# Kernel optimization log

Hardware: AMD Instinct MI355X
Metric: run time of the kernel (lower is better)

## Reference

```python
import jax, jax.numpy as jnp
import numpy as np

B, N, D, E, H = 4, 2048, 512, 16, 1024
CAP = max(4, min(N, int(N * 2.0 / E)))   # eval capacity_factor = 2.0 -> 256
EPS = 1e-9
THRESH = 0.2  # second_threshold_eval


def setup_inputs() -> dict:
    key = jax.random.key(0)
    ks = jax.random.split(key, 10)
    f32 = jnp.float32
    return {
        "X": jax.random.normal(ks[0], (B, N, D), f32),
        "probs": jax.random.uniform(ks[1], (B, N), f32),
        "W1": jax.random.normal(ks[2], (D, D), f32) * (1.0 / np.sqrt(D)),
        "b1": jnp.zeros((D,), f32),
        "Wg": jax.random.normal(ks[3], (D, E), f32),  # Top2Gating uses randn init
        "We1": jax.random.normal(ks[4], (E, D, H), f32) * (1.0 / np.sqrt(D)),
        "We2": jax.random.normal(ks[5], (E, H, D), f32) * (1.0 / np.sqrt(H)),
        "W3": jax.random.normal(ks[6], (D, 4), f32) * (1.0 / np.sqrt(D)),
        "b3": jnp.zeros((4,), f32),
        "W4": jax.random.normal(ks[7], (4, 1), f32) * 0.5,
        "b4": jnp.zeros((1,), f32),
    }


def top2_gating(x, Wg, probs):
    # x: [B, N, D] -> raw gates [B, N, E]
    raw = jax.nn.softmax(jnp.einsum('bnd,de->bne', x, Wg), axis=-1)
    dt = raw.dtype

    gate1 = jnp.max(raw, axis=-1)
    idx1 = jnp.argmax(raw, axis=-1)
    mask1 = jax.nn.one_hot(idx1, E, dtype=dt)
    density_proxy = raw

    raw_wo1 = raw * (1.0 - mask1)
    gate2 = jnp.max(raw_wo1, axis=-1)
    idx2 = jnp.argmax(raw_wo1, axis=-1)
    mask2 = jax.nn.one_hot(idx2, E, dtype=dt)

    denom = gate1 + gate2 + EPS
    gate1 = gate1 / denom
    gate2 = gate2 / denom

    # load-balancing loss (computed but wrapper discards it)
    density1 = jnp.mean(mask1, axis=-2)
    loss = jnp.mean(jnp.mean(density_proxy, axis=-2) * density1) * float(E ** 2)

    # second policy == 'random'
    mask2 = mask2 * (probs < (gate2 / max(THRESH, EPS))).astype(dt)[..., None]

    # exclusive cumsum along the group dim gives position within each expert
    pos1 = (jnp.cumsum(mask1, axis=-2) - mask1) * mask1          # [B, N, E]
    mask1 = mask1 * (pos1 < float(CAP)).astype(dt)
    mask1_count = jnp.sum(mask1, axis=-2, keepdims=True)
    mask1_flat = jnp.sum(mask1, axis=-1)                          # [B, N]
    pos1_flat = jnp.sum(pos1, axis=-1)
    gate1 = gate1 * mask1_flat

    pos2 = ((jnp.cumsum(mask2, axis=-2) - mask2) + mask1_count) * mask2
    mask2 = mask2 * (pos2 < float(CAP)).astype(dt)
    mask2_flat = jnp.sum(mask2, axis=-1)
    pos2_flat = jnp.sum(pos2, axis=-1)
    gate2 = gate2 * mask2_flat

    # safe one-hot: out-of-range positions map to all-zeros (jax.nn.one_hot semantics)
    oh_p1 = jax.nn.one_hot(pos1_flat.astype(jnp.int32), CAP, dtype=dt)
    oh_p2 = jax.nn.one_hot(pos2_flat.astype(jnp.int32), CAP, dtype=dt)
    oh_e1 = jax.nn.one_hot(idx1, E, dtype=dt)
    oh_e2 = jax.nn.one_hot(idx2, E, dtype=dt)

    combine = ((gate1 * mask1_flat)[..., None, None] * oh_e1[..., :, None] * oh_p1[..., None, :]
               + (gate2 * mask2_flat)[..., None, None] * oh_e2[..., :, None] * oh_p2[..., None, :])
    dispatch = (combine != 0).astype(dt)
    return dispatch, combine, loss


def reference(X, probs, W1, b1, Wg, We1, We2, W3, b3, W4, b4):
    h = X @ W1 + b1                                              # linear1
    dispatch, combine, loss = top2_gating(h, Wg, probs)
    exp_in = jnp.einsum('bnd,bnec->ebcd', h, dispatch)           # dispatch
    hid = jax.nn.leaky_relu(jnp.einsum('ebcd,edh->ebch', exp_in, We1))
    exp_out = jnp.einsum('ebch,ehd->ebcd', hid, We2)             # experts
    moe_out = jnp.einsum('bnec,ebcd->bnd', combine, exp_out)     # combine
    out = (moe_out @ W3 + b3) @ W4 + b4                          # hidden3 -> act3
    return out
```

## Files before the change

kernel.cpp:

```cpp
#include <hip/hip_runtime.h>
#include <hip/hip_bf16.h>

#define NB 4
#define NN 2048
#define ND 512
#define NE 16
#define NH 1024
#define CAP 256
#define NTOK (NB*NN)

typedef __attribute__((ext_vector_type(8))) short bf16x8;
typedef __attribute__((ext_vector_type(4))) float f32x4;
typedef __attribute__((ext_vector_type(8))) unsigned short u16x8;

__device__ __forceinline__ void gload16(const void* gsrc, void* lds) {
    __builtin_amdgcn_global_load_lds((const __attribute__((address_space(1))) void*)gsrc,
                                     (__attribute__((address_space(3))) void*)lds, 16, 0, 0);
}
__device__ __forceinline__ unsigned short f2bf(float f) {
    union { __hip_bfloat16 b; unsigned short u; } v; v.b = __float2bfloat16(f); return v.u;
}

__global__ __launch_bounds__(256) void prep_kernel(const float* __restrict__ W1,
                                                   const float* __restrict__ Wg,
                                                   unsigned short* __restrict__ W1B,
                                                   float* __restrict__ WcT,
                                                   float* __restrict__ zbuf) {
    const int tid = threadIdx.x;
    int bid = blockIdx.x;
    if (bid < 128) {
        const int w = tid >> 6, l = tid & 63;
        const int d = bid * 4 + w;
        float a0 = 0.f, a1 = 0.f, a2 = 0.f, a3 = 0.f, a4 = 0.f, a5 = 0.f, a6 = 0.f, a7 = 0.f;
        float a8 = 0.f, a9 = 0.f, aA = 0.f, aB = 0.f, aC = 0.f, aD = 0.f, aE = 0.f, aF = 0.f;
        #pragma unroll
        for (int ch = 0; ch < 8; ++ch) {
            float x = W1[(size_t)d * ND + ch * 64 + l];
            const float4* wg4 = (const float4*)(Wg + (size_t)(ch * 64 + l) * NE);
            float4 g0 = wg4[0], g1 = wg4[1], g2 = wg4[2], g3 = wg4[3];
            a0 = fmaf(x, g0.x, a0); a1 = fmaf(x, g0.y, a1); a2 = fmaf(x, g0.z, a2); a3 = fmaf(x, g0.w, a3);
            a4 = fmaf(x, g1.x, a4); a5 = fmaf(x, g1.y, a5); a6 = fmaf(x, g1.z, a6); a7 = fmaf(x, g1.w, a7);
            a8 = fmaf(x, g2.x, a8); a9 = fmaf(x, g2.y, a9); aA = fmaf(x, g2.z, aA); aB = fmaf(x, g2.w, aB);
            aC = fmaf(x, g3.x, aC); aD = fmaf(x, g3.y, aD); aE = fmaf(x, g3.z, aE); aF = fmaf(x, g3.w, aF);
        }
        float accs[16] = {a0, a1, a2, a3, a4, a5, a6, a7, a8, a9, aA, aB, aC, aD, aE, aF};
        #pragma unroll
        for (int off = 32; off >= 1; off >>= 1)
            #pragma unroll
            for (int e = 0; e < 16; ++e) accs[e] += __shfl_xor(accs[e], off);
        #pragma unroll
        for (int e = 0; e < 16; ++e)
            if (l == e) WcT[e * ND + d] = accs[e];
        return;
    }
    bid -= 128;
    {
        if (bid == 0) zbuf[tid] = 0.f;
        int dblk = bid >> 1, hblk = bid & 1;
        const float* src = W1 + (size_t)(dblk * 64) * ND + hblk * 256 + tid;
        unsigned short* dst = W1B + (size_t)(dblk * 512 + hblk * 256 + tid) * 64;
        float v[64];
        #pragma unroll
        for (int j = 0; j < 64; ++j) v[j] = src[(size_t)j * ND];
        #pragma unroll
        for (int q = 0; q < 8; ++q) {
            u16x8 o;
            #pragma unroll
            for (int j = 0; j < 8; ++j) o[j] = f2bf(v[q * 8 + j]);
            *(u16x8*)(dst + q * 8) = o;
        }
    }
}

__global__ __launch_bounds__(256) void gating_kernel(const float* __restrict__ X,
                                                     const float* __restrict__ WcT,
                                                     const float* __restrict__ probs,
                                                     unsigned short* __restrict__ Xbf,
                                                     int* __restrict__ idx1a, int* __restrict__ idx2a,
                                                     float* __restrict__ g1a, float* __restrict__ g2a,
                                                     int* __restrict__ pos1a, int* __restrict__ pos2a) {
    __shared__ float wc[NE * ND];
    const int tid = threadIdx.x;
    #pragma unroll
    for (int i = 0; i < 32; ++i) wc[tid + 256 * i] = WcT[tid + 256 * i];
    __syncthreads();
    const int w = tid >> 6, l = tid & 63;
    const float4* wc4 = (const float4*)wc;
    for (int j = 0; j < 4; ++j) {
        int tok = blockIdx.x * 16 + j * 4 + w;
        const float4* xrow = (const float4*)(X + (size_t)tok * ND);
        float4 x0 = xrow[l], x1 = xrow[l + 64];
        {
            ushort4 o0, o1;
            o0.x = f2bf(x0.x); o0.y = f2bf(x0.y); o0.z = f2bf(x0.z); o0.w = f2bf(x0.w);
            o1.x = f2bf(x1.x); o1.y = f2bf(x1.y); o1.z = f2bf(x1.z); o1.w = f2bf(x1.w);
            *(ushort4*)(Xbf + (size_t)tok * ND + 4 * l) = o0;
            *(ushort4*)(Xbf + (size_t)tok * ND + 256 + 4 * l) = o1;
        }
        float acc[NE];
        #pragma unroll
        for (int e = 0; e < NE; ++e) {
            float4 w0 = wc4[e * 128 + l], w1 = wc4[e * 128 + l + 64];
            acc[e] = x0.x * w0.x + x0.y * w0.y + x0.z * w0.z + x0.w * w0.w
                   + x1.x * w1.x + x1.y * w1.y + x1.z * w1.z + x1.w * w1.w;
        }
        #pragma unroll
        for (int off = 32; off >= 1; off >>= 1)
            #pragma unroll
            for (int e = 0; e < NE; ++e) acc[e] += __shfl_xor(acc[e], off);

        if (l == 0) {
            float m = acc[0];
            #pragma unroll
            for (int e = 1; e < NE; ++e) m = fmaxf(m, acc[e]);
            float raw[NE]; float s = 0.f;
            #pragma unroll
            for (int e = 0; e < NE; ++e) { raw[e] = expf(acc[e] - m); s += raw[e]; }
            #pragma unroll
            for (int e = 0; e < NE; ++e) raw[e] = raw[e] / s;
            int i1 = 0; float g1 = raw[0];
            #pragma unroll
            for (int e = 1; e < NE; ++e) if (raw[e] > g1) { g1 = raw[e]; i1 = e; }
            int i2 = -1; float g2 = -1.f;
            #pragma unroll
            for (int e = 0; e < NE; ++e) if (e != i1 && raw[e] > g2) { g2 = raw[e]; i2 = e; }
            float denom = g1 + g2 + 1e-9f;
            float g1n = g1 / denom, g2n = g2 / denom;
            bool flag = probs[tok] < (g2n / 0.2f);
            idx1a[tok] = i1;
            idx2a[tok] = flag ? i2 : -1;
            g1a[tok] = g1n;
            g2a[tok] = g2n;
            pos1a[tok] = -1;
            pos2a[tok] = -1;
        }
    }
}

__global__ __launch_bounds__(512) void scan_linear1_kernel(const int* __restrict__ idx1a,
                                                           const int* __restrict__ idx2a,
                                                           int* __restrict__ pos1a, int* __restrict__ pos2a,
                                                           int* __restrict__ slot_token,
                                                           const unsigned short* __restrict__ Xbf,
                                                           const unsigned short* __restrict__ W1B,
                                                           const float* __restrict__ b1,
                                                           unsigned short* __restrict__ hbf,
                                                           const float* __restrict__ We1,
                                                           unsigned short* __restrict__ We1B,
                                                           const float* __restrict__ We2,
                                                           const float* __restrict__ W3,
                                                           const float* __restrict__ W4,
                                                           float* __restrict__ u) {
    __shared__ char smem[65536];
    const int tid = threadIdx.x;
    const int w = tid >> 6, l = tid & 63;
    if (blockIdx.x < 64) {
        const int bb = blockIdx.x;
        const int b = bb >> 4, e = bb & 15;
        int* cnt1 = (int*)smem;
        int* cnt2 = cnt1 + 8;
        int* slot = slot_token + (e * NB + b) * CAP;
        const unsigned long long below = (l == 0) ? 0ull : ((1ull << l) - 1ull);
        const int base0 = w * 256;
        int c1 = 0, c2 = 0;
        #pragma unroll
        for (int it = 0; it < 4; ++it) {
            int n = base0 + it * 64 + l;
            c1 += __popcll(__ballot(idx1a[b * NN + n] == e));
            c2 += __popcll(__ballot(idx2a[b * NN + n] == e));
        }
        if (l == 0) { cnt1[w] = c1; cnt2[w] = c2; }
        __syncthreads();
        int b1c = 0, t1 = 0, b2c = 0, t2 = 0;
        #pragma unroll
        for (int i = 0; i < 8; ++i) {
            int v1 = cnt1[i], v2 = cnt2[i];
            if (i < w) { b1c += v1; b2c += v2; }
            t1 += v1; t2 += v2;
        }
        const int start2 = (t1 < CAP) ? t1 : CAP;
        int c = b1c;
        #pragma unroll
        for (int it = 0; it < 4; ++it) {
            int n = base0 + it * 64 + l;
            bool p = (idx1a[b * NN + n] == e);
            unsigned long long m = __ballot(p);
            int pre = __popcll(m & below);
            if (p) { int pos = c + pre; if (pos < CAP) { slot[pos] = n; pos1a[b * NN + n] = pos; } }
            c += __popcll(m);
        }
        c = start2 + b2c;
        #pragma unroll
        for (int it = 0; it < 4; ++it) {
            int n = base0 + it * 64 + l;
            bool p = (idx2a[b * NN + n] == e);
            unsigned long long m = __ballot(p);
            int pre = __popcll(m & below);
            if (p) { int pos = c + pre; if (pos < CAP) { slot[pos] = n; pos2a[b * NN + n] = pos; } }
            c += __popcll(m);
        }
        int nfill = start2 + t2; nfill = (nfill < CAP) ? nfill : CAP;
        for (int i = nfill + tid; i < CAP; i += 512) slot[i] = -1;
        return;
    }
    if (blockIdx.x < 320) {
        const int lb = blockIdx.x - 64;
        const int m0 = (lb >> 2) * 128, n0 = (lb & 3) * 128;
        const int wm = w >> 1, wn = w & 1;
        const int lr = l & 15, lk = l >> 4;
        char* Ash0 = smem;
        char* Bsh0 = smem + 32768;

        auto stage = [&](int Ks, int buf) {
            #pragma unroll
            for (int i = 0; i < 2; ++i) {
                int o = i * 8192 + tid * 16;
                int r = o >> 7, bb = o & 127;
                int sb = bb ^ ((r & 7) << 4);
                gload16((const char*)Xbf + ((size_t)(m0 + r) * ND + Ks * 64) * 2 + sb,
                        Ash0 + buf * 16384 + i * 8192 + w * 1024);
                gload16((const char*)W1B + ((size_t)(Ks * 512 + n0 + r) * 64) * 2 + sb,
                        Bsh0 + buf * 16384 + i * 8192 + w * 1024);
            }
        };

        f32x4 acc[2][4] = {};
        stage(0, 0);
        __syncthreads();
        for (int Ks = 0; Ks < 8; ++Ks) {
            int buf = Ks & 1;
            if (Ks < 7) stage(Ks + 1, buf ^ 1);
            #pragma unroll
            for (int k32 = 0; k32 < 2; ++k32) {
                int kb = (k32 * 32 + 8 * lk) * 2;
                bf16x8 a[2], bfr[4];
                #pragma unroll
                for (int mi = 0; mi < 2; ++mi) {
                    int row = wm * 32 + mi * 16 + lr;
                    a[mi] = *(const bf16x8*)(Ash0 + buf * 16384 + row * 128 + (kb ^ ((row & 7) << 4)));
                }
                #pragma unroll
                for (int ni = 0; ni < 4; ++ni) {
                    int row = wn * 64 + ni * 16 + lr;
                    bfr[ni] = *(const bf16x8*)(Bsh0 + buf * 16384 + row * 128 + (kb ^ ((row & 7) << 4)));
                }
                #pragma unroll
                for (int mi = 0; mi < 2; ++mi)
                    #pragma unroll
                    for (int ni = 0; ni < 4; ++ni)
                        acc[mi][ni] = __builtin_amdgcn_mfma_f32_16x16x32_bf16(a[mi], bfr[ni], acc[mi][ni], 0, 0, 0);
            }
            __syncthreads();
        }
        #pragma unroll
        for (int mi = 0; mi < 2; ++mi)
            #pragma unroll
            for (int ni = 0; ni < 4; ++ni) {
                int col = n0 + wn * 64 + ni * 16 + lr;
                float bb1 = b1[col];
                #pragma unroll
                for (int r = 0; r < 4; ++r) {
                    int m = m0 + wm * 32 + mi * 16 + lk * 4 + r;
                    hbf[(size_t)m * ND + col] = f2bf(acc[mi][ni][r] + bb1);
                }
            }
        return;
    }
    if (blockIdx.x < 576) {
        const int tb = blockIdx.x - 320;
        const int e = tb >> 4, rem = tb & 15;
        const int dblk = rem >> 1, hblk2 = rem & 1;
        const float* src = We1 + (size_t)e * ND * NH + (size_t)(dblk * 64) * NH + hblk2 * 512 + tid;
        unsigned short* dst = We1B + ((size_t)(e * 8 + dblk) * NH + hblk2 * 512 + tid) * 64;
        float v[64];
        #pragma unroll
        for (int j = 0; j < 64; ++j) v[j] = src[(size_t)j * NH];
        #pragma unroll
        for (int q = 0; q < 8; ++q) {
            u16x8 o;
            #pragma unroll
            for (int j = 0; j < 8; ++j) o[j] = f2bf(v[q * 8 + j]);
            *(u16x8*)(dst + q * 8) = o;
        }
        return;
    }
    {
        const int ub = blockIdx.x - 576;
        float* vvs = (float*)smem;
        {
            int d = tid;
            float s0 = 0.f;
            #pragma unroll
            for (int j = 0; j < 4; ++j) s0 += W3[d * 4 + j] * W4[j];
            vvs[d] = s0;
        }
        __syncthreads();
        const float4* vv4 = (const float4*)vvs;
        const float4 v0 = vv4[l], v1 = vv4[l + 64];
        float sums[8];
        #pragma unroll
        for (int i = 0; i < 8; ++i) {
            int gr = ub * 64 + w * 8 + i;
            const float4* row = (const float4*)(We2 + (size_t)gr * ND);
            float4 a0 = row[l], a1 = row[l + 64];
            sums[i] = a0.x * v0.x + a0.y * v0.y + a0.z * v0.z + a0.w * v0.w
                    + a1.x * v1.x + a1.y * v1.y + a1.z * v1.z + a1.w * v1.w;
        }
        #pragma unroll
        for (int off = 32; off >= 1; off >>= 1)
            #pragma unroll
            for (int i = 0; i < 8; ++i) sums[i] += __shfl_xor(sums[i], off);
        if (l == 0) {
            int gr0 = ub * 64 + w * 8;
            #pragma unroll
            for (int i = 0; i < 8; ++i) u[gr0 + i] = sums[i];
        }
    }
}

__global__ __launch_bounds__(512) void expert_mfma_kernel(const unsigned short* __restrict__ hbf,
                                                          const unsigned short* __restrict__ We1B,
                                                          const float* __restrict__ u,
                                                          const int* __restrict__ slot_token,
                                                          const float* __restrict__ zbuf,
                                                          float* __restrict__ s_slot) {
    __shared__ char Ash[65536];
    __shared__ char Bsh[2][32768];
    __shared__ float u_lds[NH];
    __shared__ float sbuf[8][32];
    __shared__ int toks[64];
    const int tid = threadIdx.x;
    const int w = tid >> 6, l = tid & 63;
    const int wm = w >> 2, wn = w & 3;
    const int lr = l & 15, lk = l >> 4;
    const int bid = blockIdx.x;
    const int e = (bid & 7) | ((bid >> 7) << 3);
    const int chunk = (bid >> 3) & 15;
    const int b = chunk >> 2, c0 = (chunk & 3) * 64;

    if (tid < 64) toks[tid] = slot_token[(e * NB + b) * CAP + c0 + tid];
    u_lds[tid] = u[e * NH + tid];
    u_lds[tid + 512] = u[e * NH + tid + 512];
    __syncthreads();
    #pragma unroll
    for (int i = 0; i < 8; ++i) {
        int r = i * 8 + w;
        int t = toks[r];
        int sb = (l * 16) ^ ((r & 7) << 4);
        const char* src = (t >= 0) ? ((const char*)hbf + ((size_t)(b * NN + t) * ND) * 2 + sb)
                                   : ((const char*)zbuf + sb);
        gload16(src, Ash + i * 8192 + w * 1024);
    }
    auto stageB = [&](int s, int buf) {
        int Hc = s >> 3, Ks = s & 7;
        #pragma unroll
        for (int i = 0; i < 4; ++i) {
            int o = i * 8192 + tid * 16;
            int r = o >> 7, bb = o & 127;
            int sb = bb ^ ((r & 7) << 4);
            gload16((const char*)We1B + (((size_t)(e * 8 + Ks) * NH + Hc * 256 + r) * 64) * 2 + sb,
                    Bsh[buf] + i * 8192 + w * 1024);
        }
    };
    f32x4 acc[2][4] = {};
    float srow[2][4] = {};
    stageB(0, 0);
    __syncthreads();
    for (int s = 0; s < 32; ++s) {
        int buf = s & 1;
        if (s < 31) stageB(s + 1, buf ^ 1);
        #pragma unroll
        for (int k32 = 0; k32 < 2; ++k32) {
            int kbA = ((s & 7) * 64 + k32 * 32 + 8 * lk) * 2;
            int kbB = (k32 * 32 + 8 * lk) * 2;
            bf16x8 a[2], bfr[4];
            #pragma unroll
            for (int mi = 0; mi < 2; ++mi) {
                int row = wm * 32 + mi * 16 + lr;
                a[mi] = *(const bf16x8*)(Ash + row * 1024 + (kbA ^ ((row & 7) << 4)));
            }
            #pragma unroll
            for (int ni = 0; ni < 4; ++ni) {
                int row = wn * 64 + ni * 16 + lr;
                bfr[ni] = *(const bf16x8*)(Bsh[buf] + row * 128 + (kbB ^ ((row & 7) << 4)));
            }
            #pragma unroll
            for (int mi = 0; mi < 2; ++mi)
                #pragma unroll
                for (int ni = 0; ni < 4; ++ni)
                    acc[mi][ni] = __builtin_amdgcn_mfma_f32_16x16x32_bf16(a[mi], bfr[ni], acc[mi][ni], 0, 0, 0);
        }
        if ((s & 7) == 7) {
            int Hc = s >> 3;
            #pragma unroll
            for (int mi = 0; mi < 2; ++mi)
                #pragma unroll
                for (int ni = 0; ni < 4; ++ni) {
                    float uu = u_lds[Hc * 256 + wn * 64 + ni * 16 + lr];
                    #pragma unroll
                    for (int r = 0; r < 4; ++r) {
                        float x = acc[mi][ni][r];
                        x = (x > 0.f) ? x : 0.01f * x;
                        srow[mi][r] = fmaf(x, uu, srow[mi][r]);
                        acc[mi][ni][r] = 0.f;
                    }
                }
        }
        __syncthreads();
    }
    #pragma unroll
    for (int off = 1; off < 16; off <<= 1)
        #pragma unroll
        for (int mi = 0; mi < 2; ++mi)
            #pragma unroll
            for (int r = 0; r < 4; ++r)
                srow[mi][r] += __shfl_xor(srow[mi][r], off);
    if (lr == 0) {
        #pragma unroll
        for (int mi = 0; mi < 2; ++mi)
            #pragma unroll
            for (int r = 0; r < 4; ++r)
                sbuf[w][mi * 16 + lk * 4 + r] = srow[mi][r];
    }
    __syncthreads();
    if (tid < 64) {
        int q = tid >> 5, rl = tid & 31;
        float s = sbuf[q * 4 + 0][rl] + sbuf[q * 4 + 1][rl] + sbuf[q * 4 + 2][rl] + sbuf[q * 4 + 3][rl];
        s_slot[(e * NB + b) * CAP + c0 + tid] = s;
    }
}

__global__ __launch_bounds__(256) void final_kernel(const int* __restrict__ idx1a, const int* __restrict__ idx2a,
                                                    const int* __restrict__ pos1a, const int* __restrict__ pos2a,
                                                    const float* __restrict__ g1a, const float* __restrict__ g2a,
                                                    const float* __restrict__ s_slot,
                                                    const float* __restrict__ b3, const float* __restrict__ W4,
                                                    const float* __restrict__ b4,
                                                    float* __restrict__ out) {
    int tok = blockIdx.x * 256 + threadIdx.x;
    int b = tok >> 11;
    float c0v = 0.f;
    #pragma unroll
    for (int j = 0; j < 4; ++j) c0v += b3[j] * W4[j];
    float s = c0v + b4[0];
    int p1 = pos1a[tok];
    if (p1 >= 0) s += g1a[tok] * s_slot[(idx1a[tok] * NB + b) * CAP + p1];
    int p2 = pos2a[tok];
    if (p2 >= 0) s += g2a[tok] * s_slot[(idx2a[tok] * NB + b) * CAP + p2];
    out[tok] = s;
}

extern "C" void kernel_launch(void* const* d_in, const int* in_sizes, int n_in,
                              void* d_out, int out_size, void* d_ws, size_t ws_size,
                              hipStream_t stream) {
    const float* X    = (const float*)d_in[0];
    const float* probs= (const float*)d_in[1];
    const float* W1   = (const float*)d_in[2];
    const float* b1   = (const float*)d_in[3];
    const float* Wg   = (const float*)d_in[4];
    const float* We1  = (const float*)d_in[5];
    const float* We2  = (const float*)d_in[6];
    const float* W3   = (const float*)d_in[7];
    const float* b3   = (const float*)d_in[8];
    const float* W4   = (const float*)d_in[9];
    const float* b4   = (const float*)d_in[10];
    float* out = (float*)d_out;

    char* ws = (char*)d_ws;
    size_t off = 0;
    auto alloc = [&](size_t bytes) { void* p = ws + off; off += (bytes + 255) & ~(size_t)255; return p; };
    unsigned short* Xbf  = (unsigned short*)alloc((size_t)NTOK * ND * 2);
    unsigned short* hbf  = (unsigned short*)alloc((size_t)NTOK * ND * 2);
    unsigned short* W1B  = (unsigned short*)alloc((size_t)ND * ND * 2);
    unsigned short* We1B = (unsigned short*)alloc((size_t)NE * NH * ND * 2);
    float* WcT     = (float*)alloc(NE * ND * 4);
    float* u       = (float*)alloc(NE * NH * 4);
    float* zbuf    = (float*)alloc(1024);
    int*   idx1a   = (int*)alloc(NTOK * 4);
    int*   idx2a   = (int*)alloc(NTOK * 4);
    int*   pos1a   = (int*)alloc(NTOK * 4);
    int*   pos2a   = (int*)alloc(NTOK * 4);
    float* g1a     = (float*)alloc(NTOK * 4);
    float* g2a     = (float*)alloc(NTOK * 4);
    int*   slot_tok= (int*)alloc(NE * NB * CAP * 4);
    float* s_slot  = (float*)alloc(NE * NB * CAP * 4);
    (void)ws_size; (void)in_sizes; (void)n_in; (void)out_size;

    prep_kernel<<<144, 256, 0, stream>>>(W1, Wg, W1B, WcT, zbuf);
    gating_kernel<<<NTOK / 16, 256, 0, stream>>>(X, WcT, probs, Xbf,
                                                 idx1a, idx2a, g1a, g2a, pos1a, pos2a);
    scan_linear1_kernel<<<832, 512, 0, stream>>>(idx1a, idx2a, pos1a, pos2a, slot_tok,
                                                 Xbf, W1B, b1, hbf,
                                                 We1, We1B, We2, W3, W4, u);
    expert_mfma_kernel<<<256, 512, 0, stream>>>(hbf, We1B, u, slot_tok, zbuf, s_slot);
    final_kernel<<<NTOK / 256, 256, 0, stream>>>(idx1a, idx2a, pos1a, pos2a, g1a, g2a, s_slot, b3, W4, b4, out);
}
```

Baseline: 90.90 us.

## Fuse combine into expert kernel via atomics and retile expert GEMM

Drops the final combine kernel and the pos1/pos2/s_slot buffers. The gating kernel now writes the constant bias term into out, and the expert kernel atomically adds gate-weighted slot sums directly to each token. Slot entries tag second-choice tokens with a high bit so the right gate can be picked. The expert MFMA loop is retiled so each wave covers all 64 rows and a 64-column slice of a 512-wide H chunk. Weight-conversion and u blocks in the scan kernel each do twice the work, which cuts the grid from 832 to 576 blocks. This saves a launch and some global traffic, but adds float atomics that make the summation order nondeterministic.

```diff
diff --git a/kernel.cpp b/kernel.cpp
--- a/kernel.cpp
+++ b/kernel.cpp
@@ -75,14 +75,20 @@
 __global__ __launch_bounds__(256) void gating_kernel(const float* __restrict__ X,
                                                      const float* __restrict__ WcT,
                                                      const float* __restrict__ probs,
+                                                     const float* __restrict__ b3,
+                                                     const float* __restrict__ W4,
+                                                     const float* __restrict__ b4,
                                                      unsigned short* __restrict__ Xbf,
                                                      int* __restrict__ idx1a, int* __restrict__ idx2a,
                                                      float* __restrict__ g1a, float* __restrict__ g2a,
-                                                     int* __restrict__ pos1a, int* __restrict__ pos2a) {
+                                                     float* __restrict__ out) {
     __shared__ float wc[NE * ND];
     const int tid = threadIdx.x;
     #pragma unroll
     for (int i = 0; i < 32; ++i) wc[tid + 256 * i] = WcT[tid + 256 * i];
+    float c0v = b4[0];
+    #pragma unroll
+    for (int j = 0; j < 4; ++j) c0v += b3[j] * W4[j];
     __syncthreads();
     const int w = tid >> 6, l = tid & 63;
     const float4* wc4 = (const float4*)wc;
@@ -131,15 +137,13 @@
             idx2a[tok] = flag ? i2 : -1;
             g1a[tok] = g1n;
             g2a[tok] = g2n;
-            pos1a[tok] = -1;
-            pos2a[tok] = -1;
+            out[tok] = c0v;
         }
     }
 }
 
 __global__ __launch_bounds__(512) void scan_linear1_kernel(const int* __restrict__ idx1a,
                                                            const int* __restrict__ idx2a,
-                                                           int* __restrict__ pos1a, int* __restrict__ pos2a,
                                                            int* __restrict__ slot_token,
                                                            const unsigned short* __restrict__ Xbf,
                                                            const unsigned short* __restrict__ W1B,
@@ -186,7 +190,7 @@
             bool p = (idx1a[b * NN + n] == e);
             unsigned long long m = __ballot(p);
             int pre = __popcll(m & below);
-            if (p) { int pos = c + pre; if (pos < CAP) { slot[pos] = n; pos1a[b * NN + n] = pos; } }
+            if (p) { int pos = c + pre; if (pos < CAP) slot[pos] = n; }
             c += __popcll(m);
         }
         c = start2 + b2c;
@@ -196,7 +200,7 @@
             bool p = (idx2a[b * NN + n] == e);
             unsigned long long m = __ballot(p);
             int pre = __popcll(m & below);
-            if (p) { int pos = c + pre; if (pos < CAP) { slot[pos] = n; pos2a[b * NN + n] = pos; } }
+            if (p) { int pos = c + pre; if (pos < CAP) slot[pos] = n | (1 << 30); }
             c += __popcll(m);
         }
         int nfill = start2 + t2; nfill = (nfill < CAP) ? nfill : CAP;
@@ -266,26 +270,30 @@
             }
         return;
     }
-    if (blockIdx.x < 576) {
+    if (blockIdx.x < 448) {
         const int tb = blockIdx.x - 320;
-        const int e = tb >> 4, rem = tb & 15;
-        const int dblk = rem >> 1, hblk2 = rem & 1;
-        const float* src = We1 + (size_t)e * ND * NH + (size_t)(dblk * 64) * NH + hblk2 * 512 + tid;
-        unsigned short* dst = We1B + ((size_t)(e * 8 + dblk) * NH + hblk2 * 512 + tid) * 64;
-        float v[64];
-        #pragma unroll
-        for (int j = 0; j < 64; ++j) v[j] = src[(size_t)j * NH];
-        #pragma unroll
-        for (int q = 0; q < 8; ++q) {
-            u16x8 o;
-            #pragma unroll
-            for (int j = 0; j < 8; ++j) o[j] = f2bf(v[q * 8 + j]);
-            *(u16x8*)(dst + q * 8) = o;
+        #pragma unroll
+        for (int q2 = 0; q2 < 2; ++q2) {
+            const int unit = tb * 2 + q2;
+            const int e = unit >> 4, rem = unit & 15;
+            const int dblk = rem >> 1, hblk2 = rem & 1;
+            const float* src = We1 + (size_t)e * ND * NH + (size_t)(dblk * 64) * NH + hblk2 * 512 + tid;
+            unsigned short* dst = We1B + ((size_t)(e * 8 + dblk) * NH + hblk2 * 512 + tid) * 64;
+            float v[64];
+            #pragma unroll
+            for (int j = 0; j < 64; ++j) v[j] = src[(size_t)j * NH];
+            #pragma unroll
+            for (int q = 0; q < 8; ++q) {
+                u16x8 o;
+                #pragma unroll
+                for (int j = 0; j < 8; ++j) o[j] = f2bf(v[q * 8 + j]);
+                *(u16x8*)(dst + q * 8) = o;
+            }
         }
         return;
     }
     {
-        const int ub = blockIdx.x - 576;
+        const int ub = blockIdx.x - 448;
         float* vvs = (float*)smem;
         {
             int d = tid;
@@ -297,23 +305,26 @@
         __syncthreads();
         const float4* vv4 = (const float4*)vvs;
         const float4 v0 = vv4[l], v1 = vv4[l + 64];
-        float sums[8];
-        #pragma unroll
-        for (int i = 0; i < 8; ++i) {
-            int gr = ub * 64 + w * 8 + i;
-            const float4* row = (const float4*)(We2 + (size_t)gr * ND);
-            float4 a0 = row[l], a1 = row[l + 64];
-            sums[i] = a0.x * v0.x + a0.y * v0.y + a0.z * v0.z + a0.w * v0.w
-                    + a1.x * v1.x + a1.y * v1.y + a1.z * v1.z + a1.w * v1.w;
-        }
-        #pragma unroll
-        for (int off = 32; off >= 1; off >>= 1)
-            #pragma unroll
-            for (int i = 0; i < 8; ++i) sums[i] += __shfl_xor(sums[i], off);
-        if (l == 0) {
-            int gr0 = ub * 64 + w * 8;
-            #pragma unroll
-            for (int i = 0; i < 8; ++i) u[gr0 + i] = sums[i];
+        #pragma unroll
+        for (int pass = 0; pass < 2; ++pass) {
+            float sums[8];
+            #pragma unroll
+            for (int i = 0; i < 8; ++i) {
+                int gr = ub * 128 + pass * 64 + w * 8 + i;
+                const float4* row = (const float4*)(We2 + (size_t)gr * ND);
+                float4 a0 = row[l], a1 = row[l + 64];
+                sums[i] = a0.x * v0.x + a0.y * v0.y + a0.z * v0.z + a0.w * v0.w
+                        + a1.x * v1.x + a1.y * v1.y + a1.z * v1.z + a1.w * v1.w;
+            }
+            #pragma unroll
+            for (int off = 32; off >= 1; off >>= 1)
+                #pragma unroll
+                for (int i = 0; i < 8; ++i) sums[i] += __shfl_xor(sums[i], off);
+            if (l == 0) {
+                int gr0 = ub * 128 + pass * 64 + w * 8;
+                #pragma unroll
+                for (int i = 0; i < 8; ++i) u[gr0 + i] = sums[i];
+            }
         }
     }
 }
@@ -323,15 +334,16 @@
                                                           const float* __restrict__ u,
                                                           const int* __restrict__ slot_token,
                                                           const float* __restrict__ zbuf,
-                                                          float* __restrict__ s_slot) {
+                                                          const float* __restrict__ g1a,
+                                                          const float* __restrict__ g2a,
+                                                          float* __restrict__ out) {
     __shared__ char Ash[65536];
     __shared__ char Bsh[2][32768];
     __shared__ float u_lds[NH];
-    __shared__ float sbuf[8][32];
+    __shared__ float sbuf[8][64];
     __shared__ int toks[64];
     const int tid = threadIdx.x;
     const int w = tid >> 6, l = tid & 63;
-    const int wm = w >> 2, wn = w & 3;
     const int lr = l & 15, lk = l >> 4;
     const int bid = blockIdx.x;
     const int e = (bid & 7) | ((bid >> 7) << 3);
@@ -346,57 +358,57 @@
     for (int i = 0; i < 8; ++i) {
         int r = i * 8 + w;
         int t = toks[r];
+        int tok = t & 2047;
         int sb = (l * 16) ^ ((r & 7) << 4);
-        const char* src = (t >= 0) ? ((const char*)hbf + ((size_t)(b * NN + t) * ND) * 2 + sb)
+        const char* src = (t >= 0) ? ((const char*)hbf + ((size_t)(b * NN + tok) * ND) * 2 + sb)
                                    : ((const char*)zbuf + sb);
         gload16(src, Ash + i * 8192 + w * 1024);
     }
     auto stageB = [&](int s, int buf) {
-        int Hc = s >> 3, Ks = s & 7;
+        int Hc = s >> 4, Ks = s & 15;
+        const size_t base = ((size_t)(e * 8 + (Ks >> 1)) * NH + Hc * 512) * 64 + (Ks & 1) * 32;
         #pragma unroll
         for (int i = 0; i < 4; ++i) {
-            int o = i * 8192 + tid * 16;
-            int r = o >> 7, bb = o & 127;
-            int sb = bb ^ ((r & 7) << 4);
-            gload16((const char*)We1B + (((size_t)(e * 8 + Ks) * NH + Hc * 256 + r) * 64) * 2 + sb,
+            int r = i * 128 + w * 16 + (l >> 2);
+            int swzr = ((r >> 1) & 3) << 4;
+            int ebyte = ((l & 3) * 16) ^ swzr;
+            gload16((const char*)We1B + (base + (size_t)r * 64) * 2 + ebyte,
                     Bsh[buf] + i * 8192 + w * 1024);
         }
     };
-    f32x4 acc[2][4] = {};
-    float srow[2][4] = {};
+    f32x4 acc[4][4] = {};
+    float srow[4][4] = {};
     stageB(0, 0);
     __syncthreads();
     for (int s = 0; s < 32; ++s) {
         int buf = s & 1;
         if (s < 31) stageB(s + 1, buf ^ 1);
-        #pragma unroll
-        for (int k32 = 0; k32 < 2; ++k32) {
-            int kbA = ((s & 7) * 64 + k32 * 32 + 8 * lk) * 2;
-            int kbB = (k32 * 32 + 8 * lk) * 2;
-            bf16x8 a[2], bfr[4];
-            #pragma unroll
-            for (int mi = 0; mi < 2; ++mi) {
-                int row = wm * 32 + mi * 16 + lr;
-                a[mi] = *(const bf16x8*)(Ash + row * 1024 + (kbA ^ ((row & 7) << 4)));
-            }
+        int Ks = s & 15;
+        bf16x8 a[4], bb[4];
+        #pragma unroll
+        for (int mi = 0; mi < 4; ++mi) {
+            int row = mi * 16 + lr;
+            int kb = (Ks * 64 + lk * 16) ^ ((row & 7) << 4);
+            a[mi] = *(const bf16x8*)(Ash + row * 1024 + kb);
+        }
+        #pragma unroll
+        for (int ni = 0; ni < 4; ++ni) {
+            int row = w * 64 + ni * 16 + lr;
+            int kb = (lk * 16) ^ (((row >> 1) & 3) << 4);
+            bb[ni] = *(const bf16x8*)(Bsh[buf] + row * 64 + kb);
+        }
+        #pragma unroll
+        for (int mi = 0; mi < 4; ++mi)
+            #pragma unroll
+            for (int ni = 0; ni < 4; ++ni)
+                acc[mi][ni] = __builtin_amdgcn_mfma_f32_16x16x32_bf16(a[mi], bb[ni], acc[mi][ni], 0, 0, 0);
+        if ((s & 15) == 15) {
+            int Hc = s >> 4;
             #pragma unroll
             for (int ni = 0; ni < 4; ++ni) {
-                int row = wn * 64 + ni * 16 + lr;
-                bfr[ni] = *(const bf16x8*)(Bsh[buf] + row * 128 + (kbB ^ ((row & 7) << 4)));
-            }
-            #pragma unroll
-            for (int mi = 0; mi < 2; ++mi)
-                #pragma unroll
-                for (int ni = 0; ni < 4; ++ni)
-                    acc[mi][ni] = __builtin_amdgcn_mfma_f32_16x16x32_bf16(a[mi], bfr[ni], acc[mi][ni], 0, 0, 0);
-        }
-        if ((s & 7) == 7) {
-            int Hc = s >> 3;
-            #pragma unroll
-            for (int mi = 0; mi < 2; ++mi)
-                #pragma unroll
-                for (int ni = 0; ni < 4; ++ni) {
-                    float uu = u_lds[Hc * 256 + wn * 64 + ni * 16 + lr];
+                float uu = u_lds[Hc * 512 + w * 64 + ni * 16 + lr];
+                #pragma unroll
+                for (int mi = 0; mi < 4; ++mi)
                     #pragma unroll
                     for (int r = 0; r < 4; ++r) {
                         float x = acc[mi][ni][r];
@@ -404,50 +416,36 @@
                         srow[mi][r] = fmaf(x, uu, srow[mi][r]);
                         acc[mi][ni][r] = 0.f;
                     }
-                }
+            }
         }
         __syncthreads();
     }
     #pragma unroll
     for (int off = 1; off < 16; off <<= 1)
         #pragma unroll
-        for (int mi = 0; mi < 2; ++mi)
+        for (int mi = 0; mi < 4; ++mi)
             #pragma unroll
             for (int r = 0; r < 4; ++r)
                 srow[mi][r] += __shfl_xor(srow[mi][r], off);
     if (lr == 0) {
         #pragma unroll
-        for (int mi = 0; mi < 2; ++mi)
+        for (int mi = 0; mi < 4; ++mi)
             #pragma unroll
             for (int r = 0; r < 4; ++r)
                 sbuf[w][mi * 16 + lk * 4 + r] = srow[mi][r];
     }
     __syncthreads();
     if (tid < 64) {
-        int q = tid >> 5, rl = tid & 31;
-        float s = sbuf[q * 4 + 0][rl] + sbuf[q * 4 + 1][rl] + sbuf[q * 4 + 2][rl] + sbuf[q * 4 + 3][rl];
-        s_slot[(e * NB + b) * CAP + c0 + tid] = s;
-    }
-}
-
-__global__ __launch_bounds__(256) void final_kernel(const int* __restrict__ idx1a, const int* __restrict__ idx2a,
-                                                    const int* __restrict__ pos1a, const int* __restrict__ pos2a,
-                                                    const float* __restrict__ g1a, const float* __restrict__ g2a,
-                                                    const float* __restrict__ s_slot,
-                                                    const float* __restrict__ b3, const float* __restrict__ W4,
-                                                    const float* __restrict__ b4,
-                                                    float* __restrict__ out) {
-    int tok = blockIdx.x * 256 + threadIdx.x;
-    int b = tok >> 11;
-    float c0v = 0.f;
-    #pragma unroll
-    for (int j = 0; j < 4; ++j) c0v += b3[j] * W4[j];
-    float s = c0v + b4[0];
-    int p1 = pos1a[tok];
-    if (p1 >= 0) s += g1a[tok] * s_slot[(idx1a[tok] * NB + b) * CAP + p1];
-    int p2 = pos2a[tok];
-    if (p2 >= 0) s += g2a[tok] * s_slot[(idx2a[tok] * NB + b) * CAP + p2];
-    out[tok] = s;
+        float s = 0.f;
+        #pragma unroll
+        for (int q = 0; q < 8; ++q) s += sbuf[q][tid];
+        int v = toks[tid];
+        if (v >= 0) {
+            int tok = v & 2047;
+            float g = (v & (1 << 30)) ? g2a[b * NN + tok] : g1a[b * NN + tok];
+            atomicAdd(out + b * NN + tok, s * g);
+        }
+    }
 }
 
 extern "C" void kernel_launch(void* const* d_in, const int* in_sizes, int n_in,
@@ -478,20 +476,16 @@
     float* zbuf    = (float*)alloc(1024);
     int*   idx1a   = (int*)alloc(NTOK * 4);
     int*   idx2a   = (int*)alloc(NTOK * 4);
-    int*   pos1a   = (int*)alloc(NTOK * 4);
-    int*   pos2a   = (int*)alloc(NTOK * 4);
     float* g1a     = (float*)alloc(NTOK * 4);
     float* g2a     = (float*)alloc(NTOK * 4);
     int*   slot_tok= (int*)alloc(NE * NB * CAP * 4);
-    float* s_slot  = (float*)alloc(NE * NB * CAP * 4);
     (void)ws_size; (void)in_sizes; (void)n_in; (void)out_size;
 
     prep_kernel<<<144, 256, 0, stream>>>(W1, Wg, W1B, WcT, zbuf);
-    gating_kernel<<<NTOK / 16, 256, 0, stream>>>(X, WcT, probs, Xbf,
-                                                 idx1a, idx2a, g1a, g2a, pos1a, pos2a);
-    scan_linear1_kernel<<<832, 512, 0, stream>>>(idx1a, idx2a, pos1a, pos2a, slot_tok,
+    gating_kernel<<<NTOK / 16, 256, 0, stream>>>(X, WcT, probs, b3, W4, b4, Xbf,
+                                                 idx1a, idx2a, g1a, g2a, out);
+    scan_linear1_kernel<<<576, 512, 0, stream>>>(idx1a, idx2a, slot_tok,
                                                  Xbf, W1B, b1, hbf,
                                                  We1, We1B, We2, W3, W4, u);
-    expert_mfma_kernel<<<256, 512, 0, stream>>>(hbf, We1B, u, slot_tok, zbuf, s_slot);
-    final_kernel<<<NTOK / 256, 256, 0, stream>>>(idx1a, idx2a, pos1a, pos2a, g1a, g2a, s_slot, b3, W4, b4, out);
-}
+    expert_mfma_kernel<<<256, 512, 0, stream>>>(hbf, We1B, u, slot_tok, zbuf, g1a, g2a, out);
+}
```

After: 84.48 us. 1.08x faster.
